# Kernel optimization log

Measured on AMD Instinct MI355X. Metric: run time of the kernel, lower is better.

Reference implementation:

```python
import jax, jax.numpy as jnp
import numpy as np

HIDDEN = 2048
N_HEADS = 16
N_KV_HEADS = 4
HEAD_DIM = 128
N_REP = N_HEADS // N_KV_HEADS
BATCH = 2
SEQ = 2048
SCALE = HEAD_DIM ** -0.5
NEG = -1e9


def apply_rope(x, freqs):
    # x: (b, s, h, d); freqs: (s, d//2) angles. Interleaved-pair rotation.
    cos = jnp.cos(freqs)[None, :, None, :]
    sin = jnp.sin(freqs)[None, :, None, :]
    x1 = x[..., 0::2]
    x2 = x[..., 1::2]
    r1 = x1 * cos - x2 * sin
    r2 = x1 * sin + x2 * cos
    return jnp.stack([r1, r2], axis=-1).reshape(x.shape)


def setup_inputs() -> dict:
    key = jax.random.key(0)
    ks = jax.random.split(key, 6)
    x = jax.random.normal(ks[0], (BATCH, SEQ, HIDDEN), dtype=jnp.float32)
    wq = jax.random.normal(ks[1], (N_HEADS * HEAD_DIM, HIDDEN), dtype=jnp.float32) * 0.02
    wk = jax.random.normal(ks[2], (N_KV_HEADS * HEAD_DIM, HIDDEN), dtype=jnp.float32) * 0.02
    wv = jax.random.normal(ks[3], (N_KV_HEADS * HEAD_DIM, HIDDEN), dtype=jnp.float32) * 0.02
    wo = jax.random.normal(ks[4], (HIDDEN, N_HEADS * HEAD_DIM), dtype=jnp.float32) * 0.02
    # RoPE angle table: pos * theta^{-2i/d}
    inv_freq = 1.0 / (10000.0 ** (jnp.arange(0, HEAD_DIM, 2, dtype=jnp.float32) / HEAD_DIM))
    rope_freqs = jnp.arange(SEQ, dtype=jnp.float32)[:, None] * inv_freq[None, :]  # (S, d/2)
    # additive causal mask
    causal = jnp.tril(jnp.ones((SEQ, SEQ), dtype=bool))
    mask = jnp.where(causal, 0.0, NEG).astype(jnp.float32)[None, None]  # (1,1,S,S)
    return {"x": x, "wq": wq, "wk": wk, "wv": wv, "wo": wo,
            "rope_freqs": rope_freqs, "mask": mask}


def reference(x, wq, wk, wv, wo, rope_freqs, mask):
    b, s, _ = x.shape
    q = (x @ wq.T).reshape(b, s, N_HEADS, HEAD_DIM)
    k = (x @ wk.T).reshape(b, s, N_KV_HEADS, HEAD_DIM)
    v = (x @ wv.T).reshape(b, s, N_KV_HEADS, HEAD_DIM)
    q = apply_rope(q, rope_freqs)
    k = apply_rope(k, rope_freqs)
    new_k, new_v = k, v  # kv cache (no prior cache, start_pos=0)
    # GQA: repeat each kv head n_rep times (matches expand+reshape in source)
    k_rep = jnp.repeat(k, N_REP, axis=2)  # (b, s, n_heads, d)
    v_rep = jnp.repeat(v, N_REP, axis=2)
    scores = jnp.einsum('bqhd,bkhd->bhqk', q, k_rep) * SCALE
    scores = scores + mask
    attn = jax.nn.softmax(scores.astype(jnp.float32), axis=-1).astype(q.dtype)
    out = jnp.einsum('bhqk,bkhd->bqhd', attn, v_rep).reshape(b, s, -1)
    return out @ wo.T, (new_k, new_v)
```

## Files before the change

### kernel.cpp

```cpp
#include <hip/hip_runtime.h>
#include <hip/hip_bf16.h>

#define NH 16
#define NKV 4
#define HD 128
#define QSCALE 0.1275174272f

using bf16x8 = __attribute__((ext_vector_type(8))) __bf16;
using f32x4  = __attribute__((ext_vector_type(4))) float;
using u16x8  = __attribute__((ext_vector_type(8))) unsigned short;
using u16x4  = __attribute__((ext_vector_type(4))) unsigned short;
using u16x2  = __attribute__((ext_vector_type(2))) unsigned short;

__device__ __forceinline__ unsigned short f2b(float f) {
  __hip_bfloat16 h = __float2bfloat16(f);
  return __builtin_bit_cast(unsigned short, h);
}
__device__ __forceinline__ float b2f(unsigned short u) {
  unsigned int v = ((unsigned int)u) << 16;
  return __builtin_bit_cast(float, v);
}

__device__ __forceinline__ void glds16(const unsigned short* g, unsigned short* l) {
  __builtin_amdgcn_global_load_lds(
      (const __attribute__((address_space(1))) unsigned int*)(const void*)g,
      (__attribute__((address_space(3))) unsigned int*)(void*)l, 16, 0, 0);
}

__global__ __launch_bounds__(256) void cvt_fused(const float* __restrict__ x,
                                                 const float* __restrict__ wq,
                                                 const float* __restrict__ wk,
                                                 const float* __restrict__ wv,
                                                 const float* __restrict__ wo,
                                                 const float* __restrict__ freqs,
                                                 unsigned short* __restrict__ xb,
                                                 unsigned short* __restrict__ wqkvb,
                                                 unsigned short* __restrict__ wob,
                                                 float2* __restrict__ cs_tab) {
  int i = blockIdx.x * 256 + threadIdx.x;
  if (i >= 2359296) {
    int k = i - 2359296;
    float f = freqs[k];
    float2 cs; cs.x = cosf(f); cs.y = sinf(f);
    cs_tab[k] = cs;
    return;
  }
  const float* src;
  unsigned short* dst;
  int off;
  if (i < 1048576)      { src = x;  dst = xb;              off = i; }
  else if (i < 1572864) { src = wq; dst = wqkvb;           off = i - 1048576; }
  else if (i < 1703936) { src = wk; dst = wqkvb + 4194304; off = i - 1572864; }
  else if (i < 1835008) { src = wv; dst = wqkvb + 5242880; off = i - 1703936; }
  else                  { src = wo; dst = wob;             off = i - 1835008; }
  const float4* s4 = reinterpret_cast<const float4*>(src) + (size_t)off * 2;
  float4 v0 = s4[0], v1 = s4[1];
  u16x8 o;
  o[0] = f2b(v0.x); o[1] = f2b(v0.y); o[2] = f2b(v0.z); o[3] = f2b(v0.w);
  o[4] = f2b(v1.x); o[5] = f2b(v1.y); o[6] = f2b(v1.z); o[7] = f2b(v1.w);
  reinterpret_cast<u16x8*>(dst)[off] = o;
}

__global__ __launch_bounds__(512, 1) void gemm_qkv(const unsigned short* __restrict__ A,
                                                   const unsigned short* __restrict__ B,
                                                   const float2* __restrict__ cs_tab,
                                                   unsigned short* __restrict__ qro,
                                                   unsigned short* __restrict__ kro,
                                                   unsigned short* __restrict__ vt,
                                                   float* __restrict__ newk,
                                                   float* __restrict__ newv,
                                                   int K) {
  constexpr int BN = 384;
  constexpr int AF = 4, BF = 6, BH = 3, BL = 3;
  __shared__ unsigned short As[3][128 * 32];
  __shared__ unsigned short Bs[3][BN * 32];
  const int tid = threadIdx.x, lane = tid & 63;
  const int wid = tid >> 6, wm = wid >> 2, wn = wid & 3;
  const int cpx = gridDim.x >> 3;
  const int wgid = (blockIdx.x & 7) * cpx + (blockIdx.x >> 3);
  const int bx = wgid % 8, by = wgid / 8;
  const int row0 = by * 128, col0 = bx * BN;
  const int fr = lane & 15, g = lane >> 4;
  const int NT = K >> 5;

  size_t offA;
  {
    int cid = tid, R = cid >> 3, phys = cid & 7, cl = phys ^ (R & 7);
    offA = (size_t)(row0 + 2 * R + (cl >> 2)) * K + (cl & 3) * 8;
  }
  size_t offB[BL];
#pragma unroll
  for (int l = 0; l < BL; l++) {
    int cid = tid + l * 512, R = cid >> 3, phys = cid & 7, cl = phys ^ (R & 7);
    offB[l] = (size_t)(col0 + 2 * R + (cl >> 2)) * K + (cl & 3) * 8;
  }

  auto stage_p0 = [&](int t, int sb) {
    int k0 = t * 32;
    glds16(A + offA + k0, &As[sb][tid * 8]);
    glds16(B + offB[0] + k0, &Bs[sb][tid * 8]);
  };
  auto stage_p1 = [&](int t, int sb) {
    int k0 = t * 32;
#pragma unroll
    for (int l = 1; l < BL; l++)
      glds16(B + offB[l] + k0, &Bs[sb][(tid + l * 512) * 8]);
  };

  auto ldfrag = [&](const unsigned short* buf, int row) {
    int R = row >> 1;
    int phys = ((((row & 1) << 2) | g) ^ (R & 7));
    return *reinterpret_cast<const bf16x8*>(&buf[R * 64 + phys * 8]);
  };

  f32x4 acc[AF][BF];
#pragma unroll
  for (int i = 0; i < AF; i++)
#pragma unroll
    for (int j = 0; j < BF; j++) acc[i][j] = f32x4{0.f, 0.f, 0.f, 0.f};

  stage_p0(0, 0); stage_p1(0, 0);
  stage_p0(1, 1); stage_p1(1, 1);
  asm volatile("s_waitcnt vmcnt(4)" ::: "memory");
  __builtin_amdgcn_s_barrier();
  __builtin_amdgcn_sched_barrier(0);

  int rb = 0, sb = 2;
#pragma unroll 1
  for (int t = 0; t < NT; ++t) {
    const unsigned short* Ar = &As[rb][0];
    const unsigned short* Br = &Bs[rb][0];

    bf16x8 af[AF], bfr[BF];
#pragma unroll
    for (int mf = 0; mf < AF; mf++) af[mf] = ldfrag(Ar, wm * 64 + mf * 16 + fr);
#pragma unroll
    for (int nf = 0; nf < BH; nf++) bfr[nf] = ldfrag(Br, wn * 96 + nf * 16 + fr);
    if (t + 2 < NT) stage_p0(t + 2, sb);
    __builtin_amdgcn_s_barrier();
    asm volatile("s_waitcnt lgkmcnt(0)" ::: "memory");
    __builtin_amdgcn_sched_barrier(0);
    __builtin_amdgcn_s_setprio(1);
#pragma unroll
    for (int mf = 0; mf < AF; mf++)
#pragma unroll
      for (int nf = 0; nf < BH; nf++)
        acc[mf][nf] = __builtin_amdgcn_mfma_f32_16x16x32_bf16(af[mf], bfr[nf], acc[mf][nf], 0, 0, 0);
    __builtin_amdgcn_s_setprio(0);
    __builtin_amdgcn_sched_barrier(0);
    __builtin_amdgcn_s_barrier();

#pragma unroll
    for (int nf = BH; nf < BF; nf++) bfr[nf] = ldfrag(Br, wn * 96 + nf * 16 + fr);
    if (t + 2 < NT) stage_p1(t + 2, sb);
    __builtin_amdgcn_s_barrier();
    asm volatile("s_waitcnt lgkmcnt(0)" ::: "memory");
    __builtin_amdgcn_sched_barrier(0);
    __builtin_amdgcn_s_setprio(1);
#pragma unroll
    for (int mf = 0; mf < AF; mf++)
#pragma unroll
      for (int nf = BH; nf < BF; nf++)
        acc[mf][nf] = __builtin_amdgcn_mfma_f32_16x16x32_bf16(af[mf], bfr[nf], acc[mf][nf], 0, 0, 0);
    __builtin_amdgcn_s_setprio(0);
    __builtin_amdgcn_sched_barrier(0);

    if (t + 1 < NT) {
      if (t + 2 < NT) asm volatile("s_waitcnt vmcnt(4)" ::: "memory");
      else            asm volatile("s_waitcnt vmcnt(0)" ::: "memory");
      __builtin_amdgcn_s_barrier();
      __builtin_amdgcn_sched_barrier(0);
    }
    rb = rb == 2 ? 0 : rb + 1;
    sb = sb == 2 ? 0 : sb + 1;
  }

#pragma unroll
  for (int i = 0; i < AF; i++) {
    int rbase = row0 + wm * 64 + i * 16 + g * 4;
    int bb = rbase >> 11;
    int sr0 = rbase & 2047;
#pragma unroll
    for (int j = 0; j < BF; j++) {
      int cb = col0 + wn * 96 + j * 16 + fr;
      int d = cb & 127;
      if (cb < 2048) {
        int hq = cb >> 7;
        unsigned short* qp = qro + ((size_t)(bb * 16 + hq) * 2048 + sr0) * 128 + d;
#pragma unroll
        for (int r = 0; r < 4; r++) {
          float own = acc[i][j][r];
          float par = __shfl_xor(own, 1);
          float2 cs = cs_tab[(sr0 + r) * 64 + (d >> 1)];
          float o = (fr & 1) ? (par * cs.y + own * cs.x) : (own * cs.x - par * cs.y);
          qp[(size_t)r * 128] = f2b(o * QSCALE);
        }
      } else if (cb < 2560) {
        int kvh = (cb >> 7) & 3;
        unsigned short* kp = kro + ((size_t)(bb * 4 + kvh) * 2048 + sr0) * 128 + d;
        float* nk = newk + ((size_t)bb * 2048 + sr0) * 512 + kvh * 128 + d;
#pragma unroll
        for (int r = 0; r < 4; r++) {
          float own = acc[i][j][r];
          float par = __shfl_xor(own, 1);
          float2 cs = cs_tab[(sr0 + r) * 64 + (d >> 1)];
          float o = (fr & 1) ? (par * cs.y + own * cs.x) : (own * cs.x - par * cs.y);
          kp[(size_t)r * 128] = f2b(o);
          nk[(size_t)r * 512] = o;
        }
      } else {
        int kvh = (cb >> 7) & 3;
        float* nv = newv + ((size_t)bb * 2048 + sr0) * 512 + kvh * 128 + d;
        u16x4 pack;
#pragma unroll
        for (int r = 0; r < 4; r++) {
          float v = acc[i][j][r];
          nv[(size_t)r * 512] = v;
          pack[r] = f2b(v);
        }
        int kl = sr0 & 31;
        int slotb = ((kl >> 2) & 3) * 8 + (kl >> 4) * 4;
        *reinterpret_cast<u16x4*>(vt + ((size_t)(bb * 4 + kvh) * 128 + d) * 2048
                                  + (sr0 & ~31) + slotb) = pack;
      }
    }
  }
}

template<int CF32, int BN>
__global__ __launch_bounds__(512, 1) void gemm_full(const unsigned short* __restrict__ A,
                                                    const unsigned short* __restrict__ B,
                                                    void* __restrict__ C,
                                                    int N, int K, int nbx) {
  constexpr int BM = 128;
  constexpr int AF = 4;
  constexpr int BF = BN / 64;
  constexpr int BH = BF / 2;
  constexpr int AL = 1;
  constexpr int BL = BN / 128;
  __shared__ unsigned short As[3][BM * 32];
  __shared__ unsigned short Bs[3][BN * 32];
  const int tid = threadIdx.x, lane = tid & 63;
  const int wid = tid >> 6, wm = wid >> 2, wn = wid & 3;
  const int cpx = gridDim.x >> 3;
  const int wgid = (blockIdx.x & 7) * cpx + (blockIdx.x >> 3);
  const int bx = wgid % nbx, by = wgid / nbx;
  const int row0 = by * BM, col0 = bx * BN;
  const int fr = lane & 15, g = lane >> 4;
  const int NT = K >> 5;

  size_t offA;
  {
    int cid = tid, R = cid >> 3, phys = cid & 7, cl = phys ^ (R & 7);
    offA = (size_t)(row0 + 2 * R + (cl >> 2)) * K + (cl & 3) * 8;
  }
  size_t offB[BL];
#pragma unroll
  for (int l = 0; l < BL; l++) {
    int cid = tid + l * 512, R = cid >> 3, phys = cid & 7, cl = phys ^ (R & 7);
    offB[l] = (size_t)(col0 + 2 * R + (cl >> 2)) * K + (cl & 3) * 8;
  }

  auto stage_p0 = [&](int t, int sb) {
    int k0 = t * 32;
    glds16(A + offA + k0, &As[sb][tid * 8]);
    glds16(B + offB[0] + k0, &Bs[sb][tid * 8]);
  };
  auto stage_p1 = [&](int t, int sb) {
    int k0 = t * 32;
#pragma unroll
    for (int l = 1; l < BL; l++)
      glds16(B + offB[l] + k0, &Bs[sb][(tid + l * 512) * 8]);
  };

  auto ldfrag = [&](const unsigned short* buf, int row) {
    int R = row >> 1;
    int phys = ((((row & 1) << 2) | g) ^ (R & 7));
    return *reinterpret_cast<const bf16x8*>(&buf[R * 64 + phys * 8]);
  };

  f32x4 acc[AF][BF];
#pragma unroll
  for (int i = 0; i < AF; i++)
#pragma unroll
    for (int j = 0; j < BF; j++) acc[i][j] = f32x4{0.f, 0.f, 0.f, 0.f};

  stage_p0(0, 0); stage_p1(0, 0);
  stage_p0(1, 1); stage_p1(1, 1);
  if constexpr (AL + BL == 4) asm volatile("s_waitcnt vmcnt(4)" ::: "memory");
  else                        asm volatile("s_waitcnt vmcnt(3)" ::: "memory");
  __builtin_amdgcn_s_barrier();
  __builtin_amdgcn_sched_barrier(0);

  int rb = 0, sb = 2;
#pragma unroll 1
  for (int t = 0; t < NT; ++t) {
    const unsigned short* Ar = &As[rb][0];
    const unsigned short* Br = &Bs[rb][0];

    bf16x8 af[AF], bfr[BF];
#pragma unroll
    for (int mf = 0; mf < AF; mf++) af[mf] = ldfrag(Ar, wm * 64 + mf * 16 + fr);
#pragma unroll
    for (int nf = 0; nf < BH; nf++) bfr[nf] = ldfrag(Br, wn * (BN / 4) + nf * 16 + fr);
    if (t + 2 < NT) stage_p0(t + 2, sb);
    __builtin_amdgcn_s_barrier();
    asm volatile("s_waitcnt lgkmcnt(0)" ::: "memory");
    __builtin_amdgcn_sched_barrier(0);
    __builtin_amdgcn_s_setprio(1);
#pragma unroll
    for (int mf = 0; mf < AF; mf++)
#pragma unroll
      for (int nf = 0; nf < BH; nf++)
        acc[mf][nf] = __builtin_amdgcn_mfma_f32_16x16x32_bf16(af[mf], bfr[nf], acc[mf][nf], 0, 0, 0);
    __builtin_amdgcn_s_setprio(0);
    __builtin_amdgcn_sched_barrier(0);
    __builtin_amdgcn_s_barrier();

#pragma unroll
    for (int nf = BH; nf < BF; nf++) bfr[nf] = ldfrag(Br, wn * (BN / 4) + nf * 16 + fr);
    if (t + 2 < NT) stage_p1(t + 2, sb);
    __builtin_amdgcn_s_barrier();
    asm volatile("s_waitcnt lgkmcnt(0)" ::: "memory");
    __builtin_amdgcn_sched_barrier(0);
    __builtin_amdgcn_s_setprio(1);
#pragma unroll
    for (int mf = 0; mf < AF; mf++)
#pragma unroll
      for (int nf = BH; nf < BF; nf++)
        acc[mf][nf] = __builtin_amdgcn_mfma_f32_16x16x32_bf16(af[mf], bfr[nf], acc[mf][nf], 0, 0, 0);
    __builtin_amdgcn_s_setprio(0);
    __builtin_amdgcn_sched_barrier(0);

    if (t + 1 < NT) {
      if (t + 2 < NT) {
        if constexpr (AL + BL == 4) asm volatile("s_waitcnt vmcnt(4)" ::: "memory");
        else                        asm volatile("s_waitcnt vmcnt(3)" ::: "memory");
      } else {
        asm volatile("s_waitcnt vmcnt(0)" ::: "memory");
      }
      __builtin_amdgcn_s_barrier();
      __builtin_amdgcn_sched_barrier(0);
    }
    rb = rb == 2 ? 0 : rb + 1;
    sb = sb == 2 ? 0 : sb + 1;
  }

#pragma unroll
  for (int i = 0; i < AF; i++) {
#pragma unroll
    for (int j = 0; j < BF; j++) {
      int rbase = row0 + wm * 64 + i * 16 + g * 4;
      int cb = col0 + wn * (BN / 4) + j * 16 + fr;
#pragma unroll
      for (int r = 0; r < 4; r++) {
        if (CF32)
          reinterpret_cast<float*>(C)[(size_t)(rbase + r) * N + cb] = acc[i][j][r];
        else
          reinterpret_cast<unsigned short*>(C)[(size_t)(rbase + r) * N + cb] = f2b(acc[i][j][r]);
      }
    }
  }
}

__global__ __launch_bounds__(256, 4) void attn_kernel(const unsigned short* __restrict__ qro,
                                                      const unsigned short* __restrict__ kro,
                                                      const unsigned short* __restrict__ vt,
                                                      unsigned short* __restrict__ out) {
  __shared__ unsigned short Ks[2][32 * 128];
  __shared__ unsigned short Vs[2][64 * 64];
  const int tid = threadIdx.x, lane = tid & 63, w = tid >> 6;
  const int kvhb = blockIdx.x & 7;
  const int kvh = kvhb & 3, b = kvhb >> 2;
  const int t = 127 - (blockIdx.x >> 3);
  const int h = kvh * 4 + w;
  const int qbase = t * 16;
  const int fr = lane & 15, g = lane >> 4, fk = g * 8;
  const unsigned short* Kp = kro + (size_t)(b * 4 + kvh) * 2048 * 128;
  const unsigned short* Vtp = vt + (size_t)(b * 4 + kvh) * 128 * 2048;
  const unsigned short* Qp = qro + ((size_t)(b * 16 + h) * 2048 + qbase) * 128;

  bf16x8 qf[4];
#pragma unroll
  for (int kk = 0; kk < 4; kk++)
    qf[kk] = *reinterpret_cast<const bf16x8*>(Qp + fr * 128 + kk * 32 + fk);

  u16x8 onesu;
#pragma unroll
  for (int j = 0; j < 8; j++) onesu[j] = 0x3F80;
  bf16x8 ones = __builtin_bit_cast(bf16x8, onesu);

  f32x4 o[8];
#pragma unroll
  for (int dt = 0; dt < 8; dt++) o[dt] = f32x4{0.f, 0.f, 0.f, 0.f};
  f32x4 dacc = f32x4{0.f, 0.f, 0.f, 0.f};
  const int qrow_s = qbase + fr;
  const int nfull = (qbase >= 31) ? ((qbase - 31) >> 5) + 1 : 0;
  const int niter = nfull + 1;

  const int krow = w * 8 + (lane >> 4);
  const int kcol = lane & 15;
  const int vrow = w * 16 + (lane >> 3);
  const int vcol = lane & 7;

  auto stage = [&](int kv0, int buf) {
    unsigned short* Kb = &Ks[buf][0];
    unsigned short* Vb = &Vs[buf][0];
#pragma unroll
    for (int j = 0; j < 2; j++) {
      int r = krow + j * 4;
      glds16(Kp + (size_t)(kv0 + r) * 128 + ((kcol ^ (r & 7)) * 8),
             Kb + (w * 8 + j * 4) * 128);
    }
#pragma unroll
    for (int j = 0; j < 2; j++) {
      int r = vrow + j * 8;
      int u = vcol ^ (r & 7);
      int d = 2 * r + (u >> 2);
      glds16(Vtp + (size_t)d * 2048 + kv0 + (u & 3) * 8,
             Vb + (w * 16 + j * 8) * 64);
    }
  };

  auto step = [&](int kv0, bool mask, int buf) {
    const unsigned short* Kb = &Ks[buf][0];
    const unsigned short* Vb = &Vs[buf][0];
    f32x4 sc[2];
    sc[0] = sc[1] = f32x4{0.f, 0.f, 0.f, 0.f};
    __builtin_amdgcn_s_setprio(1);
#pragma unroll
    for (int kk = 0; kk < 4; kk++) {
      int blk = ((kk * 4 + g) ^ (fr & 7)) * 8;
      bf16x8 ka0 = *reinterpret_cast<const bf16x8*>(Kb + (fr +  0) * 128 + blk);
      bf16x8 ka1 = *reinterpret_cast<const bf16x8*>(Kb + (fr + 16) * 128 + blk);
      sc[0] = __builtin_amdgcn_mfma_f32_16x16x32_bf16(ka0, qf[kk], sc[0], 0, 0, 0);
      sc[1] = __builtin_amdgcn_mfma_f32_16x16x32_bf16(ka1, qf[kk], sc[1], 0, 0, 0);
    }
    __builtin_amdgcn_s_setprio(0);
#pragma unroll
    for (int s = 0; s < 2; s++)
#pragma unroll
      for (int r = 0; r < 4; r++) {
        float v = sc[s][r];
        if (mask && (kv0 + 16 * s + 4 * g + r > qrow_s)) v = -1e30f;
        sc[s][r] = __builtin_amdgcn_exp2f(v);
      }
    u16x8 pau;
#pragma unroll
    for (int j = 0; j < 4; j++) {
      pau[j]     = f2b(sc[0][j]);
      pau[4 + j] = f2b(sc[1][j]);
    }
    bf16x8 pa = __builtin_bit_cast(bf16x8, pau);
    dacc = __builtin_amdgcn_mfma_f32_16x16x32_bf16(pa, ones, dacc, 0, 0, 0);
    __builtin_amdgcn_s_setprio(1);
#pragma unroll
    for (int dt = 0; dt < 8; dt++) {
      int jr = dt * 8 + (fr >> 1);
      int c = ((fr & 1) * 4 + g) ^ (fr >> 1);
      bf16x8 vf = *reinterpret_cast<const bf16x8*>(Vb + jr * 64 + c * 8);
      o[dt] = __builtin_amdgcn_mfma_f32_16x16x32_bf16(pa, vf, o[dt], 0, 0, 0);
    }
    __builtin_amdgcn_s_setprio(0);
  };

  stage(0, 0);
  int buf = 0;
  for (int i = 0; i < niter; i++) {
    __syncthreads();
    if (i + 1 < niter) stage((i + 1) * 32, buf ^ 1);
    step(i * 32, i == nfull, buf);
    buf ^= 1;
  }

#pragma unroll
  for (int r = 0; r < 4; r++) {
    float inv = 1.0f / dacc[r];
    int qrow = qbase + g * 4 + r;
    size_t rowoff = ((size_t)b * 2048 + qrow) * 2048 + (size_t)h * 128;
#pragma unroll
    for (int dt = 0; dt < 8; dt++)
      out[rowoff + dt * 16 + fr] = f2b(o[dt][r] * inv);
  }
}

extern "C" void kernel_launch(void* const* d_in, const int* in_sizes, int n_in,
                              void* d_out, int out_size, void* d_ws, size_t ws_size,
                              hipStream_t stream) {
  const float* x  = (const float*)d_in[0];
  const float* wq = (const float*)d_in[1];
  const float* wk = (const float*)d_in[2];
  const float* wv = (const float*)d_in[3];
  const float* wo = (const float*)d_in[4];
  const float* freqs = (const float*)d_in[5];

  char* ws = (char*)d_ws;
  unsigned short* xb    = (unsigned short*)(ws);
  unsigned short* attn  = xb;
  unsigned short* wqkvb = (unsigned short*)(ws + 16777216);
  unsigned short* wob   = (unsigned short*)(ws + 29360128);
  float2*         cstab = (float2*)(ws + 37748736);
  unsigned short* qro   = (unsigned short*)(ws + 62914560);
  unsigned short* kro   = (unsigned short*)(ws + 79691776);
  unsigned short* vt    = (unsigned short*)(ws + 83886080);

  float* out_o = (float*)d_out;
  float* out_k = (float*)d_out + 8388608;
  float* out_v = (float*)d_out + 10485760;

  cvt_fused<<<9728, 256, 0, stream>>>(x, wq, wk, wv, wo, freqs, xb, wqkvb, wob, cstab);

  gemm_qkv<<<256, 512, 0, stream>>>(xb, wqkvb, cstab, qro, kro, vt, out_k, out_v, 2048);

  attn_kernel<<<1024, 256, 0, stream>>>(qro, kro, vt, attn);

  gemm_full<1, 256><<<256, 512, 0, stream>>>(attn, wob, out_o, 2048, 2048, 8);
}
```

Measured before the change: 195.3 us.

## Share K/V staging across two query sub-tiles per attention block

The attention block grows from 256 to 512 threads, eight waves covering two 16-row query sub-tiles for each of the four heads in a KV group. Each K/V tile loaded into LDS now serves 32 query rows instead of 16, which halves global K/V traffic and staging work per query. The grid is halved and the tile order is remapped to a mix of short and long causal tiles. In exchange, each wave has less load work to hide latency, the first sub-tile computes extra masked work in its last step, and launch_bounds(512,4) tightens the per-wave register budget, which may cause spills.

After: 195.4 us. No clear change (+0.1%).

```diff
diff --git a/kernel.cpp b/kernel.cpp
--- a/kernel.cpp
+++ b/kernel.cpp
@@ -363,7 +363,7 @@
   }
 }
 
-__global__ __launch_bounds__(256, 4) void attn_kernel(const unsigned short* __restrict__ qro,
+__global__ __launch_bounds__(512, 4) void attn_kernel(const unsigned short* __restrict__ qro,
                                                       const unsigned short* __restrict__ kro,
                                                       const unsigned short* __restrict__ vt,
                                                       unsigned short* __restrict__ out) {
@@ -372,9 +372,11 @@
   const int tid = threadIdx.x, lane = tid & 63, w = tid >> 6;
   const int kvhb = blockIdx.x & 7;
   const int kvh = kvhb & 3, b = kvhb >> 2;
-  const int t = 127 - (blockIdx.x >> 3);
-  const int h = kvh * 4 + w;
-  const int qbase = t * 16;
+  const int s = blockIdx.x >> 3;
+  const int T = (s < 32) ? s : (95 - s);
+  const int sub = w >> 2, hh = w & 3;
+  const int h = kvh * 4 + hh;
+  const int qbase = T * 32 + sub * 16;
   const int fr = lane & 15, g = lane >> 4, fk = g * 8;
   const unsigned short* Kp = kro + (size_t)(b * 4 + kvh) * 2048 * 128;
   const unsigned short* Vtp = vt + (size_t)(b * 4 + kvh) * 128 * 2048;
@@ -395,31 +397,20 @@
   for (int dt = 0; dt < 8; dt++) o[dt] = f32x4{0.f, 0.f, 0.f, 0.f};
   f32x4 dacc = f32x4{0.f, 0.f, 0.f, 0.f};
   const int qrow_s = qbase + fr;
-  const int nfull = (qbase >= 31) ? ((qbase - 31) >> 5) + 1 : 0;
-  const int niter = nfull + 1;
-
-  const int krow = w * 8 + (lane >> 4);
+  const int niter = T + 1;
+
+  const int krow = w * 4 + (lane >> 4);
   const int kcol = lane & 15;
-  const int vrow = w * 16 + (lane >> 3);
+  const int vr = w * 8 + (lane >> 3);
   const int vcol = lane & 7;
 
   auto stage = [&](int kv0, int buf) {
-    unsigned short* Kb = &Ks[buf][0];
-    unsigned short* Vb = &Vs[buf][0];
-#pragma unroll
-    for (int j = 0; j < 2; j++) {
-      int r = krow + j * 4;
-      glds16(Kp + (size_t)(kv0 + r) * 128 + ((kcol ^ (r & 7)) * 8),
-             Kb + (w * 8 + j * 4) * 128);
-    }
-#pragma unroll
-    for (int j = 0; j < 2; j++) {
-      int r = vrow + j * 8;
-      int u = vcol ^ (r & 7);
-      int d = 2 * r + (u >> 2);
-      glds16(Vtp + (size_t)d * 2048 + kv0 + (u & 3) * 8,
-             Vb + (w * 16 + j * 8) * 64);
-    }
+    glds16(Kp + (size_t)(kv0 + krow) * 128 + ((kcol ^ (krow & 7)) * 8),
+           &Ks[buf][w * 4 * 128]);
+    int u = vcol ^ (vr & 7);
+    int d = 2 * vr + (u >> 2);
+    glds16(Vtp + (size_t)d * 2048 + kv0 + (u & 3) * 8,
+           &Vs[buf][w * 8 * 64]);
   };
 
   auto step = [&](int kv0, bool mask, int buf) {
@@ -438,12 +429,12 @@
     }
     __builtin_amdgcn_s_setprio(0);
 #pragma unroll
-    for (int s = 0; s < 2; s++)
+    for (int ss = 0; ss < 2; ss++)
 #pragma unroll
       for (int r = 0; r < 4; r++) {
-        float v = sc[s][r];
-        if (mask && (kv0 + 16 * s + 4 * g + r > qrow_s)) v = -1e30f;
-        sc[s][r] = __builtin_amdgcn_exp2f(v);
+        float v = sc[ss][r];
+        if (mask && (kv0 + 16 * ss + 4 * g + r > qrow_s)) v = -1e30f;
+        sc[ss][r] = __builtin_amdgcn_exp2f(v);
       }
     u16x8 pau;
 #pragma unroll
@@ -469,7 +460,7 @@
   for (int i = 0; i < niter; i++) {
     __syncthreads();
     if (i + 1 < niter) stage((i + 1) * 32, buf ^ 1);
-    step(i * 32, i == nfull, buf);
+    step(i * 32, i == niter - 1, buf);
     buf ^= 1;
   }
 
@@ -512,7 +503,7 @@
 
   gemm_qkv<<<256, 512, 0, stream>>>(xb, wqkvb, cstab, qro, kro, vt, out_k, out_v, 2048);
 
-  attn_kernel<<<1024, 256, 0, stream>>>(qro, kro, vt, attn);
+  attn_kernel<<<512, 512, 0, stream>>>(qro, kro, vt, attn);
 
   gemm_full<1, 256><<<256, 512, 0, stream>>>(attn, wob, out_o, 2048, 2048, 8);
 }
```
